# Performance work log

Hardware: AMD Instinct MI355X
Metric: run time of the kernel (lower is better)

Reference implementation:

```python
import jax, jax.numpy as jnp
import numpy as np

B_SZ, L, D, N, H = 2, 2048, 1024, 16, 128

def celu(x):
    # F.celu with alpha=1: max(0,x) + min(0, exp(x)-1)
    return jnp.where(x > 0, x, jnp.expm1(x))

def setup_inputs() -> dict:
    key = jax.random.key(0)
    ks = jax.random.split(key, 16)
    s = lambda fan_in: 1.0 / np.sqrt(fan_in)
    inp = {
        "x": jax.random.normal(ks[0], (B_SZ, L, D), jnp.float32),
        # fc1: d->d, fc2/fc3: d->n
        "W1": jax.random.normal(ks[1], (D, D), jnp.float32) * s(D),
        "b1": jnp.zeros((D,), jnp.float32),
        "W2": jax.random.normal(ks[2], (D, N), jnp.float32) * s(D),
        "b2": jnp.zeros((N,), jnp.float32),
        "W3": jax.random.normal(ks[3], (D, N), jnp.float32) * s(D),
        "b3": jnp.zeros((N,), jnp.float32),
        # lift_fn: Linear(d,128) -> relu -> Linear(128,d) -> tanh
        "Wl1": jax.random.normal(ks[4], (D, H), jnp.float32) * s(D),
        "bl1": jnp.zeros((H,), jnp.float32),
        "Wl2": jax.random.normal(ks[5], (H, D), jnp.float32) * s(H),
        "bl2": jnp.zeros((D,), jnp.float32),
        # fc_net: Linear(2d,128) -> relu -> (dropout, eval: identity) -> Linear(128,d)
        "Wf1": jax.random.normal(ks[6], (2 * D, H), jnp.float32) * s(2 * D),
        "bf1": jnp.zeros((H,), jnp.float32),
        "Wf2": jax.random.normal(ks[7], (H, D), jnp.float32) * s(H),
        "bf2": jnp.zeros((D,), jnp.float32),
        "state_init": jnp.zeros((1, D, N), jnp.float32),
        # kaiming_normal_ on (d, n): std = sqrt(2 / fan_in), fan_in = n
        "A": jax.random.normal(ks[8], (D, N), jnp.float32) * np.sqrt(2.0 / N),
    }
    return inp

def reference(x, W1, b1, W2, b2, W3, b3, Wl1, bl1, Wl2, bl2, Wf1, bf1, Wf2, bf2, state_init, A):
    b = x.shape[0]
    # lift_fn
    lifted = jnp.tanh(jax.nn.relu(x @ Wl1 + bl1) @ Wl2 + bl2)          # [b,l,d]
    combined = jnp.concatenate([x, lifted], axis=-1)                    # [b,l,2d]
    x_trans = jax.nn.relu(combined @ Wf1 + bf1) @ Wf2 + bf2             # [b,l,d]
    h_prev = jnp.broadcast_to(state_init, (b,) + state_init.shape[1:])  # [b,d,n]
    Bm = x_trans @ W2 + b2                                              # [b,l,n]
    Cm = x_trans @ W3 + b3                                              # [b,l,n]
    delta = jax.nn.softplus(x_trans @ W1 + b1)                          # [b,l,d]
    # discretization: bldn outer products
    dB = delta[..., :, None] * Bm[..., None, :]                         # [b,l,d,n]
    dA = jnp.exp(-celu(delta[..., :, None] * A[None, None]))            # [b,l,d,n]
    h_new = dA * h_prev[:, None] + x_trans[..., None] * dB              # [b,l,d,n]
    output = jnp.einsum('bln,bldn->bld', Cm, h_new)                     # [b,l,d]
    last_h_state = h_new[:, -1]                                         # [b,d,n]
    return (output, last_h_state)
```

## Files before the change

kernel.cpp:

```cpp
#include <hip/hip_runtime.h>
#include <cmath>

#define B_SZ 2
#define LSEQ 2048
#define DDIM 1024
#define NDIM 16
#define HDIM 128
#define MROWS (B_SZ * LSEQ)
#define NBIG (DDIM + 2 * NDIM)
#define NPAD 1088

typedef __bf16 bf16x8 __attribute__((ext_vector_type(8)));
typedef __bf16 bf16x4 __attribute__((ext_vector_type(4)));
typedef float f32x4 __attribute__((ext_vector_type(4)));

__device__ __forceinline__ void glds16(const __bf16* g, __bf16* l) {
    __builtin_amdgcn_global_load_lds(
        (const __attribute__((address_space(1))) unsigned int*)g,
        (__attribute__((address_space(3))) unsigned int*)l, 16, 0, 0);
}

__device__ __forceinline__ int slot_xt(int d) { return (d >> 4) * 32 + (d & 15); }
__device__ __forceinline__ int slot_de(int d) { return (d >> 4) * 32 + 16 + (d & 15); }

__device__ __forceinline__ void tcast_tile(const float* __restrict__ in,
                                           __bf16* __restrict__ out, int K, int N,
                                           int bx, int by, float (*t)[33]) {
    int tx = threadIdx.x & 31, ty = threadIdx.x >> 5;
    int n0 = bx * 32, k0 = by * 32;
    #pragma unroll
    for (int i = 0; i < 4; ++i) {
        int k = k0 + ty + i * 8, n = n0 + tx;
        t[ty + i * 8][tx] = (k < K && n < N) ? in[(size_t)k * N + n] : 0.f;
    }
    __syncthreads();
    #pragma unroll
    for (int i = 0; i < 4; ++i) {
        int n = n0 + ty + i * 8, k = k0 + tx;
        if (n < N && k < K) out[(size_t)n * K + k] = (__bf16)t[tx][ty + i * 8];
    }
}

__device__ __forceinline__ void tcast_pair_tile(const float* __restrict__ in,
                                                __bf16* __restrict__ out,
                                                int bx, int by, float (*t)[33]) {
    int tx = threadIdx.x & 31, ty = threadIdx.x >> 5;
    int n0 = bx * 32, k0 = by * 32;
    #pragma unroll
    for (int i = 0; i < 4; ++i) {
        int k = k0 + ty + i * 8, n = n0 + tx;
        t[ty + i * 8][tx] = in[(size_t)k * 1024 + n];
    }
    __syncthreads();
    #pragma unroll
    for (int i = 0; i < 4; ++i) {
        int n = n0 + ty + i * 8, k = k0 + tx;
        out[(size_t)slot_xt(n) * 128 + k] = (__bf16)t[tx][ty + i * 8];
    }
}

__global__ __launch_bounds__(256) void pack_all(
    const float* W1, const float* W2, const float* W3, const float* Wl1,
    const float* Wl2, const float* Wf1, const float* Wf2,
    const float* bf2, const float* h0,
    __bf16* WbigT, __bf16* WaT, __bf16* Wf1bT, __bf16* Wl2T, __bf16* WpairT,
    __bf16* Wf2c, float* bias_pair, unsigned* h0mask) {
    __shared__ float t[32][33];
    const int b = blockIdx.x;
    const int tid = threadIdx.x;
    if (b < 1024) {
        tcast_tile(W1, WbigT, 1024, 1024, b & 31, b >> 5, t);
    } else if (b < 1152) {
        int i = b - 1024; tcast_tile(Wl1, WaT, 1024, 128, i & 3, i >> 2, t);
    } else if (b < 1280) {
        int i = b - 1152; tcast_tile(Wf1, WaT + 128 * 1024, 1024, 128, i & 3, i >> 2, t);
    } else if (b < 1408) {
        int i = b - 1280;
        tcast_tile(Wf1 + (size_t)1024 * 128, Wf1bT, 1024, 128, i & 3, i >> 2, t);
    } else if (b < 1536) {
        int i = b - 1408; tcast_tile(Wl2, Wl2T, 128, 1024, i & 31, i >> 5, t);
    } else if (b < 1664) {
        int i = b - 1536; tcast_pair_tile(Wf2, WpairT, i & 31, i >> 5, t);
    } else if (b < 1696) {
        int i = b - 1664; tcast_tile(W2, WbigT + (size_t)1024 * 1024, 1024, 16, 0, i, t);
    } else if (b < 1728) {
        int i = b - 1696; tcast_tile(W3, WbigT + (size_t)1040 * 1024, 1024, 16, 0, i, t);
    } else if (b < 1732) {
        int i = (b - 1728) * 256 + tid;
        bias_pair[slot_xt(i)] = bf2[i];
    } else if (b < 1764) {
        int i = (b - 1732) * 256 + tid;
        #pragma unroll
        for (int r = 0; r < 4; ++r) {
            int e = i + r * 8192;
            if (e < 32 * 1024) WbigT[(size_t)1056 * 1024 + e] = (__bf16)0.f;
        }
    } else if (b < 1796) {
        int id = (b - 1764) * 256 + tid;
        #pragma unroll
        for (int j = 0; j < 4; ++j) {
            int e = id + j * 8192;
            float4 v = ((const float4*)Wf2)[e];
            bf16x4 o2 = {(__bf16)v.x, (__bf16)v.y, (__bf16)v.z, (__bf16)v.w};
            ((bf16x4*)Wf2c)[e] = o2;
        }
    } else {
        __shared__ unsigned sm[32];
        if (tid < 32) sm[tid] = 0u;
        __syncthreads();
        unsigned nib = 0;
        #pragma unroll
        for (int j = 0; j < 4; ++j) {
            int d = tid * 4 + j;
            const uint4* hu = (const uint4*)(h0 + d * NDIM);
            uint4 a0 = hu[0], a1 = hu[1], a2 = hu[2], a3 = hu[3];
            unsigned nz = a0.x | a0.y | a0.z | a0.w | a1.x | a1.y | a1.z | a1.w |
                          a2.x | a2.y | a2.z | a2.w | a3.x | a3.y | a3.z | a3.w;
            if (nz) nib |= (1u << j);
        }
        if (nib) atomicOr(&sm[(tid * 4) >> 5], nib << ((tid * 4) & 31));
        __syncthreads();
        if (tid < 32) h0mask[tid] = sm[tid];
    }
}

template <int BM, int BN, int ACT, bool ADD_PREV, bool GUARDN, bool AF32>
__device__ __forceinline__ void gemm_core(
    const void* Av, int lda, const __bf16* __restrict__ Bt, int ldb, int Ntot,
    const float* __restrict__ bias, const __bf16* __restrict__ prev, int ldp,
    __bf16* __restrict__ C, int ldc, int K, int bm, int bn,
    __bf16* As, __bf16* Bs) {
    constexpr int WM = BM / 2, WN = BN / 2, FM = WM / 16, FN = WN / 16;
    constexpr int ASZ = BM * 64, BSZ = BN * 64;
    const int tid = threadIdx.x;
    const int lane = tid & 63, w = tid >> 6;
    const int wr = w >> 1, wc = w & 1;
    const int g = lane >> 4, lr = lane & 15;
    const __bf16* A16 = (const __bf16*)Av;
    const float* A32 = (const float*)Av;

    auto stage = [&](int buf, int k0) {
        #pragma unroll
        for (int i = 0; i < BM / 32; ++i) {
            int D = i * 256 + tid;
            int row = D >> 3, pos = D & 7, c = pos ^ (row & 7);
            if constexpr (AF32) {
                const float* s = &A32[(size_t)(bm + row) * lda + k0 + c * 8];
                float4 v0 = *(const float4*)s;
                float4 v1 = *(const float4*)(s + 4);
                bf16x8 pk = {(__bf16)v0.x, (__bf16)v0.y, (__bf16)v0.z, (__bf16)v0.w,
                             (__bf16)v1.x, (__bf16)v1.y, (__bf16)v1.z, (__bf16)v1.w};
                *(bf16x8*)&As[buf * ASZ + row * 64 + pos * 8] = pk;
            } else {
                glds16(&A16[(size_t)(bm + row) * lda + k0 + c * 8],
                       &As[buf * ASZ + (i * 256 + w * 64) * 8]);
            }
        }
        #pragma unroll
        for (int i = 0; i < BN / 32; ++i) {
            int D = i * 256 + tid;
            int row = D >> 3, pos = D & 7, c = pos ^ (row & 7);
            glds16(&Bt[(size_t)(bn + row) * ldb + k0 + c * 8],
                   &Bs[buf * BSZ + (i * 256 + w * 64) * 8]);
        }
    };

    f32x4 acc[FM][FN] = {};
    const int x7 = lr & 7;
    const int ca[2] = {(g ^ x7) * 8, ((4 + g) ^ x7) * 8};
    const int arow0 = wr * WM + lr;
    const int brow0 = wc * WN + lr;

    const int nt = K >> 6;
    stage(0, 0);
    __syncthreads();
    for (int t = 0; t < nt; ++t) {
        if (t + 1 < nt) stage((t + 1) & 1, (t + 1) << 6);
        const __bf16* Ab = &As[(t & 1) * ASZ];
        const __bf16* Bb = &Bs[(t & 1) * BSZ];
        bf16x8 af[FM][2], bfr[FN][2];
        #pragma unroll
        for (int m = 0; m < FM; ++m)
            #pragma unroll
            for (int h = 0; h < 2; ++h)
                af[m][h] = *(const bf16x8*)&Ab[(arow0 + m * 16) * 64 + ca[h]];
        #pragma unroll
        for (int n = 0; n < FN; ++n)
            #pragma unroll
            for (int h = 0; h < 2; ++h)
                bfr[n][h] = *(const bf16x8*)&Bb[(brow0 + n * 16) * 64 + ca[h]];
        #pragma unroll
        for (int h = 0; h < 2; ++h)
            #pragma unroll
            for (int m = 0; m < FM; ++m)
                #pragma unroll
                for (int n = 0; n < FN; ++n)
                    acc[m][n] = __builtin_amdgcn_mfma_f32_16x16x32_bf16(
                        af[m][h], bfr[n][h], acc[m][n], 0, 0, 0);
        __syncthreads();
    }

    #pragma unroll
    for (int m = 0; m < FM; ++m) {
        #pragma unroll
        for (int n = 0; n < FN; ++n) {
            #pragma unroll
            for (int r = 0; r < 4; ++r) {
                int grow = bm + wr * WM + m * 16 + g * 4 + r;
                int gcol = bn + wc * WN + n * 16 + lr;
                if (!GUARDN || gcol < Ntot) {
                    float v = acc[m][n][r];
                    int orow = grow;
                    if (ACT == 1) {
                        v += bias[gcol];
                        if (ADD_PREV) v += (float)prev[(size_t)grow * ldp + gcol];
                        v = fmaxf(v, 0.f);
                    } else if (ACT == 2) {
                        v += bias[gcol];
                        float e = __expf(2.f * v);
                        v = 1.f - 2.f * __builtin_amdgcn_rcpf(e + 1.f);
                    } else if (ACT == 4) {
                        if (gcol < HDIM) v = fmaxf(v + bias[gcol], 0.f);
                    } else if (ACT == 7) {
                        orow = (grow < 1024) ? slot_de(grow) : 2048 + (grow - 1024);
                    }
                    C[(size_t)orow * ldc + gcol] = (__bf16)v;
                }
            }
        }
    }
}

template <int BM, int BN, int ACT, bool ADD_PREV, bool GUARDN>
__global__ __launch_bounds__(256) void mm(const __bf16* __restrict__ A, int lda,
                                          const __bf16* __restrict__ Bt, int ldb, int Ntot,
                                          const float* __restrict__ bias,
                                          const __bf16* __restrict__ prev, int ldp,
                                          __bf16* __restrict__ C, int ldc, int K, int nbx) {
    __shared__ __bf16 As[2 * BM * 64];
    __shared__ __bf16 Bs[2 * BN * 64];
    const int NB = gridDim.x;
    const int aid = ((NB & 7) == 0)
                        ? (blockIdx.x & 7) * (NB >> 3) + (blockIdx.x >> 3)
                        : blockIdx.x;
    const int bn = (aid % nbx) * BN, bm = (aid / nbx) * BM;
    gemm_core<BM, BN, ACT, ADD_PREV, GUARDN, false>(
        A, lda, Bt, ldb, Ntot, bias, prev, ldp, C, ldc, K, bm, bn, As, Bs);
}

__global__ __launch_bounds__(256) void stage2_k(
    const float* __restrict__ x, const __bf16* __restrict__ WaT,
    const __bf16* __restrict__ WbigT, const __bf16* __restrict__ Wf2c,
    const float* __restrict__ bf2, const float* __restrict__ b1,
    const float* __restrict__ b2, const float* __restrict__ b3,
    const float* __restrict__ bl1,
    __bf16* __restrict__ tmp12, __bf16* __restrict__ WpairT,
    float* __restrict__ bias_pair) {
    __shared__ __bf16 As[2 * 64 * 64];
    __shared__ __bf16 Bs[2 * 64 * 64];
    const int b = blockIdx.x;
    if (b < 512) {
        const int aid = (b & 7) * 64 + (b >> 3);
        const int bn = (aid & 3) * 64, bm = (aid >> 2) * 32;
        gemm_core<32, 64, 4, false, false, true>(
            x, DDIM, WaT, 1024, 256, bl1, nullptr, 0, tmp12, 256, 1024, bm, bn, As, Bs);
    } else if (b < 546) {
        const int aid = b - 512;
        const int bn = (aid & 1) * 64, bm = (aid >> 1) * 64;
        gemm_core<64, 64, 7, false, false, false>(
            WbigT, 1024, Wf2c, 1024, 128, nullptr, nullptr, 0,
            WpairT, 128, 1024, bm, bn, As, Bs);
    } else {
        const int n = (b - 546) * 4 + (threadIdx.x >> 6);
        const int lane = threadIdx.x & 63;
        const __bf16* wr = WbigT + (size_t)n * 1024 + lane * 16;
        float s = 0.f;
        #pragma unroll
        for (int i = 0; i < 2; ++i) {
            bf16x8 wv = *(const bf16x8*)&wr[i * 8];
            float4 f0 = *(const float4*)&bf2[lane * 16 + i * 8];
            float4 f1 = *(const float4*)&bf2[lane * 16 + i * 8 + 4];
            s += (float)wv[0] * f0.x + (float)wv[1] * f0.y + (float)wv[2] * f0.z +
                 (float)wv[3] * f0.w + (float)wv[4] * f1.x + (float)wv[5] * f1.y +
                 (float)wv[6] * f1.z + (float)wv[7] * f1.w;
        }
        #pragma unroll
        for (int off = 32; off; off >>= 1) s += __shfl_down(s, off);
        if (lane == 0) {
            float base = (n < DDIM) ? b1[n]
                       : (n < DDIM + NDIM) ? b2[n - DDIM] : b3[n - DDIM - NDIM];
            int sl = (n < DDIM) ? slot_de(n) : 2048 + (n - DDIM);
            bias_pair[sl] = base + s;
        }
    }
}

__global__ __launch_bounds__(256) void bc_k(const __bf16* __restrict__ tmp2,
                                            const __bf16* __restrict__ WbcT,
                                            const float* __restrict__ bias_bc,
                                            __bf16* __restrict__ Bmv,
                                            __bf16* __restrict__ Cmv,
                                            float* __restrict__ cbv) {
    __shared__ __bf16 t2[16][128];
    const int blk = blockIdx.x, tid = threadIdx.x;
    const int rr = tid >> 4, cc = tid & 15;
    *(bf16x8*)&t2[rr][cc * 8] =
        *(const bf16x8*)&tmp2[(size_t)(blk * 16 + rr) * 128 + cc * 8];
    __syncthreads();
    float sB = bias_bc[cc], sC = bias_bc[16 + cc];
    #pragma unroll
    for (int i = 0; i < 16; ++i) {
        bf16x8 tv = *(const bf16x8*)&t2[rr][i * 8];
        bf16x8 wb = *(const bf16x8*)&WbcT[(size_t)cc * 128 + i * 8];
        bf16x8 wc2 = *(const bf16x8*)&WbcT[(size_t)(16 + cc) * 128 + i * 8];
        #pragma unroll
        for (int j = 0; j < 8; ++j) {
            float tvf = (float)tv[j];
            sB += tvf * (float)wb[j];
            sC += tvf * (float)wc2[j];
        }
    }
    const int row = blk * 16 + rr;
    Bmv[row * NDIM + cc] = (__bf16)sB;
    Cmv[row * NDIM + cc] = (__bf16)sC;
    float p = sB * sC;
    #pragma unroll
    for (int m2 = 1; m2 < 16; m2 <<= 1) p += __shfl_xor(p, m2);
    if (cc == 0) cbv[row] = p;
}

__global__ __launch_bounds__(256) void mm_pairs(
    const __bf16* __restrict__ tmp2, const __bf16* __restrict__ WpairT,
    const float* __restrict__ bias_pair, const float* __restrict__ cbv,
    const __bf16* __restrict__ Bmv, const __bf16* __restrict__ Cmv,
    const float* __restrict__ Amat, const float* __restrict__ h0,
    const unsigned* __restrict__ h0mask,
    float* __restrict__ out, float* __restrict__ last_h) {
    constexpr int ASZ = 128 * 64, BSZ = 64 * 64;
    __shared__ __bf16 As[2 * ASZ];
    __shared__ __bf16 Bs[2 * BSZ];
    const int NB = gridDim.x;
    const int aid = (blockIdx.x & 7) * (NB >> 3) + (blockIdx.x >> 3);
    const int bn = (aid & 31) * 64, bm = (aid >> 5) * 128;
    const int tid = threadIdx.x;
    const int lane = tid & 63, w = tid >> 6;
    const int wr = w >> 1, wc = w & 1;
    const int g = lane >> 4, lr = lane & 15;

    auto stage = [&](int buf, int k0) {
        #pragma unroll
        for (int i = 0; i < 4; ++i) {
            int D = i * 256 + tid;
            int row = D >> 3, pos = D & 7, c = pos ^ (row & 7);
            glds16(&tmp2[(size_t)(bm + row) * 128 + k0 + c * 8],
                   &As[buf * ASZ + (i * 256 + w * 64) * 8]);
        }
        #pragma unroll
        for (int i = 0; i < 2; ++i) {
            int D = i * 256 + tid;
            int row = D >> 3, pos = D & 7, c = pos ^ (row & 7);
            glds16(&WpairT[(size_t)(bn + row) * 128 + k0 + c * 8],
                   &Bs[buf * BSZ + (i * 256 + w * 64) * 8]);
        }
    };

    f32x4 acc[4][2] = {};
    const int x7 = lr & 7;
    const int ca[2] = {(g ^ x7) * 8, ((4 + g) ^ x7) * 8};
    const int arow0 = wr * 64 + lr, brow0 = wc * 32 + lr;
    stage(0, 0);
    __syncthreads();
    #pragma unroll
    for (int t = 0; t < 2; ++t) {
        if (t == 0) stage(1, 64);
        const __bf16* Ab = &As[t * ASZ];
        const __bf16* Bb = &Bs[t * BSZ];
        bf16x8 af[4][2], bfr[2][2];
        #pragma unroll
        for (int m = 0; m < 4; ++m)
            #pragma unroll
            for (int h = 0; h < 2; ++h)
                af[m][h] = *(const bf16x8*)&Ab[(arow0 + m * 16) * 64 + ca[h]];
        #pragma unroll
        for (int n = 0; n < 2; ++n)
            #pragma unroll
            for (int h = 0; h < 2; ++h)
                bfr[n][h] = *(const bf16x8*)&Bb[(brow0 + n * 16) * 64 + ca[h]];
        #pragma unroll
        for (int h = 0; h < 2; ++h)
            #pragma unroll
            for (int m = 0; m < 4; ++m)
                #pragma unroll
                for (int n = 0; n < 2; ++n)
                    acc[m][n] = __builtin_amdgcn_mfma_f32_16x16x32_bf16(
                        af[m][h], bfr[n][h], acc[m][n], 0, 0, 0);
        __syncthreads();
    }

    const int d = ((bn + wc * 32) >> 1) + lr;
    const float bx_ = bias_pair[bn + wc * 32 + lr];
    const float bd_ = bias_pair[bn + wc * 32 + 16 + lr];
    const bool msk = (h0mask[d >> 5] >> (d & 31)) & 1u;
    #pragma unroll
    for (int m = 0; m < 4; ++m) {
        #pragma unroll
        for (int r = 0; r < 4; ++r) {
            const int row = bm + wr * 64 + m * 16 + g * 4 + r;
            const float xt = acc[m][0][r] + bx_;
            const float dr = acc[m][1][r] + bd_;
            const float e = __expf(-fabsf(dr));
            const float de = fmaxf(dr, 0.f) + __logf(1.f + e);
            const float xd = xt * de;
            float res = xd * cbv[row];
            const bool is_last = (row & (LSEQ - 1)) == (LSEQ - 1);
            if (msk) {
                float s = 0.f;
                #pragma unroll
                for (int n = 0; n < NDIM; ++n) {
                    float z = de * Amat[d * NDIM + n];
                    float c2 = (z > 0.f) ? z : __expf(z) - 1.f;
                    float da = __expf(-c2);
                    float h0v = h0[d * NDIM + n];
                    s += (float)Cmv[row * NDIM + n] * da * h0v;
                    if (is_last)
                        last_h[(((size_t)(row >> 11)) * DDIM + d) * NDIM + n] =
                            da * h0v + xd * (float)Bmv[row * NDIM + n];
                }
                res += s;
            } else if (is_last) {
                #pragma unroll
                for (int n = 0; n < NDIM; ++n)
                    last_h[(((size_t)(row >> 11)) * DDIM + d) * NDIM + n] =
                        xd * (float)Bmv[row * NDIM + n];
            }
            out[(size_t)row * DDIM + d] = res;
        }
    }
}

extern "C" void kernel_launch(void* const* d_in, const int* in_sizes, int n_in,
                              void* d_out, int out_size, void* d_ws, size_t ws_size,
                              hipStream_t stream) {
    const float* x   = (const float*)d_in[0];
    const float* W1  = (const float*)d_in[1];
    const float* b1  = (const float*)d_in[2];
    const float* W2  = (const float*)d_in[3];
    const float* b2  = (const float*)d_in[4];
    const float* W3  = (const float*)d_in[5];
    const float* b3  = (const float*)d_in[6];
    const float* Wl1 = (const float*)d_in[7];
    const float* bl1 = (const float*)d_in[8];
    const float* Wl2 = (const float*)d_in[9];
    const float* bl2 = (const float*)d_in[10];
    const float* Wf1 = (const float*)d_in[11];
    const float* bf1 = (const float*)d_in[12];
    const float* Wf2 = (const float*)d_in[13];
    const float* bf2 = (const float*)d_in[14];
    const float* h0  = (const float*)d_in[15];
    const float* Amat= (const float*)d_in[16];

    float* out    = (float*)d_out;
    float* last_h = (float*)d_out + (size_t)MROWS * DDIM;

    __bf16* wsb = (__bf16*)d_ws;
    size_t o = 0;
    auto alloc = [&](size_t n) { __bf16* p = wsb + o; o += n; return p; };
    __bf16* WaT    = alloc(256 * 1024);
    __bf16* Wf1bT  = alloc(128 * 1024);
    __bf16* Wl2T   = alloc(1024 * 128);
    __bf16* WbigT  = alloc((size_t)NPAD * 1024);
    __bf16* WpairT = alloc(2112 * 128);
    __bf16* Wf2c   = alloc(128 * 1024);
    __bf16* tmp12  = alloc((size_t)MROWS * 256);
    __bf16* lifted = alloc((size_t)MROWS * DDIM);
    __bf16* tmp2   = alloc((size_t)MROWS * HDIM);
    __bf16* Bmv    = alloc((size_t)MROWS * NDIM);
    __bf16* Cmv    = alloc((size_t)MROWS * NDIM);
    float*  bias_pair = (float*)(wsb + o); o += 2 * 2112;
    float*  cbv    = (float*)(wsb + o); o += 2 * MROWS;
    unsigned* h0mask = (unsigned*)(wsb + o);

    pack_all<<<dim3(1797), 256, 0, stream>>>(W1, W2, W3, Wl1, Wl2, Wf1, Wf2,
                                             bf2, h0,
                                             WbigT, WaT, Wf1bT, Wl2T, WpairT,
                                             Wf2c, bias_pair, h0mask);
    stage2_k<<<dim3(810), 256, 0, stream>>>(x, WaT, WbigT, Wf2c, bf2, b1, b2, b3,
                                            bl1, tmp12, WpairT, bias_pair);
    mm<64, 64, 2, false, false><<<dim3(16 * 64), 256, 0, stream>>>(
        tmp12, 256, Wl2T, 128, 1024, bl2, nullptr, 0, lifted, DDIM, 128, 16);
    mm<32, 32, 1, true, false><<<dim3(4 * 128), 256, 0, stream>>>(
        lifted, DDIM, Wf1bT, 1024, 128, bf1, tmp12 + 128, 256, tmp2, HDIM, 1024, 4);
    bc_k<<<dim3(MROWS / 16), 256, 0, stream>>>(tmp2, WpairT + 2048 * 128,
                                               bias_pair + 2048, Bmv, Cmv, cbv);
    mm_pairs<<<dim3(32 * 32), 256, 0, stream>>>(tmp2, WpairT, bias_pair, cbv,
                                                Bmv, Cmv, Amat, h0, h0mask,
                                                out, last_h);
}
```

Measured before the change: 59.10 us.

## Fuse B/C projection into mm_pairs epilogue using MFMA on resident A tile

Removes the separate bc_k kernel, which computed Bm, Cm and their dot product per row. mm_pairs now loads the 32 B/C weight rows into LDS after its main loop and computes them with MFMA from the tmp2 tile already resident in shared memory, keeping the results in LDS for the epilogue. This drops one launch and the global round-trip of Bmv, Cmv and cbv. In exchange each of the 32 column blocks recomputes the same B/C values for its row tile, and extra syncs and LDS traffic are added before the epilogue.

```diff
diff --git a/kernel.cpp b/kernel.cpp
--- a/kernel.cpp
+++ b/kernel.cpp
@@ -295,44 +295,9 @@
     }
 }
 
-__global__ __launch_bounds__(256) void bc_k(const __bf16* __restrict__ tmp2,
-                                            const __bf16* __restrict__ WbcT,
-                                            const float* __restrict__ bias_bc,
-                                            __bf16* __restrict__ Bmv,
-                                            __bf16* __restrict__ Cmv,
-                                            float* __restrict__ cbv) {
-    __shared__ __bf16 t2[16][128];
-    const int blk = blockIdx.x, tid = threadIdx.x;
-    const int rr = tid >> 4, cc = tid & 15;
-    *(bf16x8*)&t2[rr][cc * 8] =
-        *(const bf16x8*)&tmp2[(size_t)(blk * 16 + rr) * 128 + cc * 8];
-    __syncthreads();
-    float sB = bias_bc[cc], sC = bias_bc[16 + cc];
-    #pragma unroll
-    for (int i = 0; i < 16; ++i) {
-        bf16x8 tv = *(const bf16x8*)&t2[rr][i * 8];
-        bf16x8 wb = *(const bf16x8*)&WbcT[(size_t)cc * 128 + i * 8];
-        bf16x8 wc2 = *(const bf16x8*)&WbcT[(size_t)(16 + cc) * 128 + i * 8];
-        #pragma unroll
-        for (int j = 0; j < 8; ++j) {
-            float tvf = (float)tv[j];
-            sB += tvf * (float)wb[j];
-            sC += tvf * (float)wc2[j];
-        }
-    }
-    const int row = blk * 16 + rr;
-    Bmv[row * NDIM + cc] = (__bf16)sB;
-    Cmv[row * NDIM + cc] = (__bf16)sC;
-    float p = sB * sC;
-    #pragma unroll
-    for (int m2 = 1; m2 < 16; m2 <<= 1) p += __shfl_xor(p, m2);
-    if (cc == 0) cbv[row] = p;
-}
-
 __global__ __launch_bounds__(256) void mm_pairs(
     const __bf16* __restrict__ tmp2, const __bf16* __restrict__ WpairT,
-    const float* __restrict__ bias_pair, const float* __restrict__ cbv,
-    const __bf16* __restrict__ Bmv, const __bf16* __restrict__ Cmv,
+    const float* __restrict__ bias_pair,
     const float* __restrict__ Amat, const float* __restrict__ h0,
     const unsigned* __restrict__ h0mask,
     float* __restrict__ out, float* __restrict__ last_h) {
@@ -397,6 +362,51 @@
         __syncthreads();
     }
 
+    {
+        int row = tid >> 3, pos = tid & 7, c = pos ^ (row & 7);
+        #pragma unroll
+        for (int t2 = 0; t2 < 2; ++t2)
+            glds16(&WpairT[(size_t)(2048 + row) * 128 + t2 * 64 + c * 8],
+                   &Bs[t2 * 2048 + w * 512]);
+    }
+    __syncthreads();
+    f32x4 accB[2] = {}, accC[2] = {};
+    #pragma unroll
+    for (int t2 = 0; t2 < 2; ++t2) {
+        const __bf16* Ab = &As[t2 * ASZ];
+        #pragma unroll
+        for (int h = 0; h < 2; ++h) {
+            bf16x8 bB = *(const bf16x8*)&Bs[t2 * 2048 + lr * 64 + ca[h]];
+            bf16x8 bC = *(const bf16x8*)&Bs[t2 * 2048 + (16 + lr) * 64 + ca[h]];
+            #pragma unroll
+            for (int m2 = 0; m2 < 2; ++m2) {
+                bf16x8 a2 = *(const bf16x8*)&Ab[(w * 32 + m2 * 16 + lr) * 64 + ca[h]];
+                accB[m2] = __builtin_amdgcn_mfma_f32_16x16x32_bf16(a2, bB, accB[m2], 0, 0, 0);
+                accC[m2] = __builtin_amdgcn_mfma_f32_16x16x32_bf16(a2, bC, accC[m2], 0, 0, 0);
+            }
+        }
+    }
+    __syncthreads();
+    float* sCB = (float*)As;
+    __bf16* sBC = &Bs[BSZ];
+    const float bB_ = bias_pair[2048 + lr], bC_ = bias_pair[2064 + lr];
+    #pragma unroll
+    for (int m2 = 0; m2 < 2; ++m2) {
+        #pragma unroll
+        for (int r = 0; r < 4; ++r) {
+            int lrow = w * 32 + m2 * 16 + g * 4 + r;
+            float vB = accB[m2][r] + bB_;
+            float vC = accC[m2][r] + bC_;
+            sBC[lrow * 32 + lr] = (__bf16)vB;
+            sBC[lrow * 32 + 16 + lr] = (__bf16)vC;
+            float p = vB * vC;
+            #pragma unroll
+            for (int m3 = 1; m3 < 16; m3 <<= 1) p += __shfl_xor(p, m3);
+            if (lr == 0) sCB[lrow] = p;
+        }
+    }
+    __syncthreads();
+
     const int d = ((bn + wc * 32) >> 1) + lr;
     const float bx_ = bias_pair[bn + wc * 32 + lr];
     const float bd_ = bias_pair[bn + wc * 32 + 16 + lr];
@@ -405,13 +415,14 @@
     for (int m = 0; m < 4; ++m) {
         #pragma unroll
         for (int r = 0; r < 4; ++r) {
-            const int row = bm + wr * 64 + m * 16 + g * 4 + r;
+            const int lrow = wr * 64 + m * 16 + g * 4 + r;
+            const int row = bm + lrow;
             const float xt = acc[m][0][r] + bx_;
             const float dr = acc[m][1][r] + bd_;
             const float e = __expf(-fabsf(dr));
             const float de = fmaxf(dr, 0.f) + __logf(1.f + e);
             const float xd = xt * de;
-            float res = xd * cbv[row];
+            float res = xd * sCB[lrow];
             const bool is_last = (row & (LSEQ - 1)) == (LSEQ - 1);
             if (msk) {
                 float s = 0.f;
@@ -421,17 +432,17 @@
                     float c2 = (z > 0.f) ? z : __expf(z) - 1.f;
                     float da = __expf(-c2);
                     float h0v = h0[d * NDIM + n];
-                    s += (float)Cmv[row * NDIM + n] * da * h0v;
+                    s += (float)sBC[lrow * 32 + 16 + n] * da * h0v;
                     if (is_last)
                         last_h[(((size_t)(row >> 11)) * DDIM + d) * NDIM + n] =
-                            da * h0v + xd * (float)Bmv[row * NDIM + n];
+                            da * h0v + xd * (float)sBC[lrow * 32 + n];
                 }
                 res += s;
             } else if (is_last) {
                 #pragma unroll
                 for (int n = 0; n < NDIM; ++n)
                     last_h[(((size_t)(row >> 11)) * DDIM + d) * NDIM + n] =
-                        xd * (float)Bmv[row * NDIM + n];
+                        xd * (float)sBC[lrow * 32 + n];
             }
             out[(size_t)row * DDIM + d] = res;
         }
@@ -474,10 +485,7 @@
     __bf16* tmp12  = alloc((size_t)MROWS * 256);
     __bf16* lifted = alloc((size_t)MROWS * DDIM);
     __bf16* tmp2   = alloc((size_t)MROWS * HDIM);
-    __bf16* Bmv    = alloc((size_t)MROWS * NDIM);
-    __bf16* Cmv    = alloc((size_t)MROWS * NDIM);
     float*  bias_pair = (float*)(wsb + o); o += 2 * 2112;
-    float*  cbv    = (float*)(wsb + o); o += 2 * MROWS;
     unsigned* h0mask = (unsigned*)(wsb + o);
 
     pack_all<<<dim3(1797), 256, 0, stream>>>(W1, W2, W3, Wl1, Wl2, Wf1, Wf2,
@@ -490,9 +498,6 @@
         tmp12, 256, Wl2T, 128, 1024, bl2, nullptr, 0, lifted, DDIM, 128, 16);
     mm<32, 32, 1, true, false><<<dim3(4 * 128), 256, 0, stream>>>(
         lifted, DDIM, Wf1bT, 1024, 128, bf1, tmp12 + 128, 256, tmp2, HDIM, 1024, 4);
-    bc_k<<<dim3(MROWS / 16), 256, 0, stream>>>(tmp2, WpairT + 2048 * 128,
-                                               bias_pair + 2048, Bmv, Cmv, cbv);
-    mm_pairs<<<dim3(32 * 32), 256, 0, stream>>>(tmp2, WpairT, bias_pair, cbv,
-                                                Bmv, Cmv, Amat, h0, h0mask,
-                                                out, last_h);
-}
+    mm_pairs<<<dim3(32 * 32), 256, 0, stream>>>(tmp2, WpairT, bias_pair,
+                                                Amat, h0, h0mask, out, last_h);
+}
```

Measured after the change: 56.41 us. -4.5%, faster.
